# Kernel tuning notes

Hardware: AMD Instinct MI355X
Metric: run time of the kernel (lower is better)

Reference implementation:

```python
import jax, jax.numpy as jnp
import numpy as np

BATCH, C, BOX = 8, 1, 160
N, L = 20, 20


def setup_inputs() -> dict:
    key = jax.random.key(0)
    k1, k2, k3 = jax.random.split(key, 3)
    x = jax.random.normal(k1, (BATCH, C, BOX, BOX), dtype=jnp.float32)
    basis = jax.random.normal(k2, (N, L, 2, BOX, BOX), dtype=jnp.float32)
    angles = jax.random.uniform(k3, (BATCH,), dtype=jnp.float32) * (2.0 * np.pi)
    return {"x": x, "basis": basis, "angles": angles}


def reference(x, basis, angles):
    # euclid2basis: linear basis projection (GEMM in disguise)
    # coeffs: [b, c, N, L, 2]
    coeffs = jnp.einsum('bcij,nlrij->bcnlr', x, basis)

    # rotate: complex rotation of angular modes, angle scaled by harmonic index l
    l_mult = jnp.arange(L, dtype=x.dtype)                  # [L]
    ang = angles[:, None, None, None] * l_mult             # [b, 1, 1, L]
    ca, sa = jnp.cos(ang), jnp.sin(ang)
    a = coeffs[..., 0] * ca + coeffs[..., 1] * sa
    b = coeffs[..., 1] * ca - coeffs[..., 0] * sa
    rot = jnp.stack([a, b], axis=-1)                       # [b, c, N, L, 2]

    # basis2euclid: reconstruction (transpose GEMM)
    out = jnp.einsum('bcnlr,nlrij->bcij', rot, basis)      # [b, c, H, W]
    return out
```

## Files before the change

kernel.cpp:

```cpp
#include <hip/hip_runtime.h>
#include <math.h>

#define BATCH   8
#define LDIM    20
#define PIX     25600
#define PIX4    6400
#define NLPAIRS 400
#define NLR     800

#define NLG     2
#define KSPLIT  5
#define SLICE   (PIX4 / KSPLIT)

#define RPIX    64
#define RKS     4
#define RKLEN   (NLR / RKS)

__global__ __launch_bounds__(256) void proj_kernel(
    const float* __restrict__ x,
    const float* __restrict__ basis,
    float* __restrict__ part)
{
    const int tid   = threadIdx.x;
    const int rbase = blockIdx.x * (NLG * 2);
    const int kbase = blockIdx.y * SLICE;

    const float4* __restrict__ r0 = (const float4*)(basis + (size_t)(rbase + 0) * PIX);
    const float4* __restrict__ r1 = (const float4*)(basis + (size_t)(rbase + 1) * PIX);
    const float4* __restrict__ r2 = (const float4*)(basis + (size_t)(rbase + 2) * PIX);
    const float4* __restrict__ r3 = (const float4*)(basis + (size_t)(rbase + 3) * PIX);
    const float4* __restrict__ x4 = (const float4*)x;

    float acc[4][BATCH];
    #pragma unroll
    for (int r = 0; r < 4; ++r)
        #pragma unroll
        for (int b = 0; b < BATCH; ++b) acc[r][b] = 0.0f;

    #pragma unroll
    for (int it = 0; it < SLICE / 256; ++it) {
        const int i = kbase + it * 256 + tid;
        float4 b0 = r0[i];
        float4 b1 = r1[i];
        float4 b2 = r2[i];
        float4 b3 = r3[i];
        #pragma unroll
        for (int b = 0; b < BATCH; ++b) {
            float4 xv = x4[(size_t)b * PIX4 + i];
            acc[0][b] = fmaf(b0.x, xv.x, acc[0][b]);
            acc[0][b] = fmaf(b0.y, xv.y, acc[0][b]);
            acc[0][b] = fmaf(b0.z, xv.z, acc[0][b]);
            acc[0][b] = fmaf(b0.w, xv.w, acc[0][b]);
            acc[1][b] = fmaf(b1.x, xv.x, acc[1][b]);
            acc[1][b] = fmaf(b1.y, xv.y, acc[1][b]);
            acc[1][b] = fmaf(b1.z, xv.z, acc[1][b]);
            acc[1][b] = fmaf(b1.w, xv.w, acc[1][b]);
            acc[2][b] = fmaf(b2.x, xv.x, acc[2][b]);
            acc[2][b] = fmaf(b2.y, xv.y, acc[2][b]);
            acc[2][b] = fmaf(b2.z, xv.z, acc[2][b]);
            acc[2][b] = fmaf(b2.w, xv.w, acc[2][b]);
            acc[3][b] = fmaf(b3.x, xv.x, acc[3][b]);
            acc[3][b] = fmaf(b3.y, xv.y, acc[3][b]);
            acc[3][b] = fmaf(b3.z, xv.z, acc[3][b]);
            acc[3][b] = fmaf(b3.w, xv.w, acc[3][b]);
        }
    }

    #pragma unroll
    for (int r = 0; r < 4; ++r)
        #pragma unroll
        for (int b = 0; b < BATCH; ++b)
            #pragma unroll
            for (int off = 32; off > 0; off >>= 1)
                acc[r][b] += __shfl_down(acc[r][b], off);

    __shared__ float red[4][32];
    const int wave = tid >> 6;
    const int lane = tid & 63;
    if (lane == 0) {
        #pragma unroll
        for (int r = 0; r < 4; ++r)
            #pragma unroll
            for (int b = 0; b < BATCH; ++b)
                red[wave][r * BATCH + b] = acc[r][b];
    }
    __syncthreads();

    if (tid < 32) {
        const int r = tid >> 3;
        const int b = tid & 7;
        float v = red[0][tid] + red[1][tid] + red[2][tid] + red[3][tid];
        part[((size_t)blockIdx.y * NLR + rbase + r) * BATCH + b] = v;
    }
}

__global__ __launch_bounds__(256) void recon_kernel(
    const float* __restrict__ basis,
    const float* __restrict__ part,
    const float* __restrict__ angles,
    float* __restrict__ out)
{
    __shared__ float rl[NLR * BATCH];
    __shared__ float red[RKS - 1][RPIX][BATCH];
    __shared__ float cst[LDIM * BATCH], snt[LDIM * BATCH];

    const int tid = threadIdx.x;

    if (tid < LDIM * BATCH) {
        const int l = tid >> 3;
        const int b = tid & 7;
        __sincosf(angles[b] * (float)l, &snt[tid], &cst[tid]);
    }
    __syncthreads();

    for (int idx = tid; idx < NLR * BATCH; idx += 256) {
        const int nlr = idx >> 3;
        const int b   = idx & 7;
        float self = 0.0f, other = 0.0f;
        #pragma unroll
        for (int s = 0; s < KSPLIT; ++s) {
            self  += part[((size_t)s * NLR + nlr) * BATCH + b];
            other += part[((size_t)s * NLR + (nlr ^ 1)) * BATCH + b];
        }
        const int l  = (nlr >> 1) % LDIM;
        const float ca = cst[l * BATCH + b];
        const float sa = snt[l * BATCH + b];
        rl[idx] = (nlr & 1) == 0 ? fmaf(self, ca, other * sa)
                                 : fmaf(self, ca, -other * sa);
    }
    __syncthreads();

    const int lane = tid & 63;
    const int ks   = tid >> 6;
    const int pix  = blockIdx.x * RPIX + lane;

    float acc[BATCH];
    #pragma unroll
    for (int b = 0; b < BATCH; ++b) acc[b] = 0.0f;

    const float* __restrict__ bp = basis + (size_t)(ks * RKLEN) * PIX + pix;
    const float* __restrict__ rp = &rl[(ks * RKLEN) * BATCH];

    #pragma unroll 10
    for (int k = 0; k < RKLEN; ++k) {
        float bv = bp[(size_t)k * PIX];
        float4 v0 = *(const float4*)&rp[k * BATCH];
        float4 v1 = *(const float4*)&rp[k * BATCH + 4];
        acc[0] = fmaf(bv, v0.x, acc[0]);
        acc[1] = fmaf(bv, v0.y, acc[1]);
        acc[2] = fmaf(bv, v0.z, acc[2]);
        acc[3] = fmaf(bv, v0.w, acc[3]);
        acc[4] = fmaf(bv, v1.x, acc[4]);
        acc[5] = fmaf(bv, v1.y, acc[5]);
        acc[6] = fmaf(bv, v1.z, acc[6]);
        acc[7] = fmaf(bv, v1.w, acc[7]);
    }

    if (ks > 0) {
        #pragma unroll
        for (int b = 0; b < BATCH; ++b)
            red[ks - 1][lane][b] = acc[b];
    }
    __syncthreads();

    if (ks == 0) {
        #pragma unroll
        for (int w = 0; w < RKS - 1; ++w)
            #pragma unroll
            for (int b = 0; b < BATCH; ++b)
                acc[b] += red[w][lane][b];
        #pragma unroll
        for (int b = 0; b < BATCH; ++b)
            out[(size_t)b * PIX + pix] = acc[b];
    }
}

extern "C" void kernel_launch(void* const* d_in, const int* in_sizes, int n_in,
                              void* d_out, int out_size, void* d_ws, size_t ws_size,
                              hipStream_t stream) {
    (void)in_sizes; (void)n_in; (void)ws_size; (void)out_size;

    const float* x      = (const float*)d_in[0];
    const float* basis  = (const float*)d_in[1];
    const float* angles = (const float*)d_in[2];
    float* out  = (float*)d_out;
    float* part = (float*)d_ws;

    proj_kernel<<<dim3(NLPAIRS / NLG, KSPLIT), dim3(256), 0, stream>>>(x, basis, part);
    recon_kernel<<<dim3(PIX / RPIX), dim3(256), 0, stream>>>(basis, part, angles, out);
}
```

Baseline: 42.12 us.

## Split rotation into its own kernel and widen recon K-split to 8 waves

Moves the partial-sum reduction and the sincos rotation out of the reconstruction kernel into a small separate kernel, so each of the 400 recon blocks no longer redoes that work; recon blocks now just copy the rotated coefficients into shared memory. The recon kernel doubles to 512 threads with an 8-way K split for more memory-level parallelism, and the shared reduction buffer is transposed to avoid bank conflicts. In exchange it adds an extra kernel launch and a global round-trip for the rotated coefficients.

```diff
diff --git a/kernel.cpp b/kernel.cpp
--- a/kernel.cpp
+++ b/kernel.cpp
@@ -13,7 +13,7 @@
 #define SLICE   (PIX4 / KSPLIT)
 
 #define RPIX    64
-#define RKS     4
+#define RKS     8
 #define RKLEN   (NLR / RKS)
 
 __global__ __launch_bounds__(256) void proj_kernel(
@@ -94,40 +94,40 @@
     }
 }
 
-__global__ __launch_bounds__(256) void recon_kernel(
-    const float* __restrict__ basis,
+__global__ __launch_bounds__(256) void rotate_kernel(
     const float* __restrict__ part,
     const float* __restrict__ angles,
+    float* __restrict__ rot)
+{
+    const int idx = blockIdx.x * 256 + threadIdx.x;
+    const int nlr = idx >> 3;
+    const int b   = idx & 7;
+
+    float self = 0.0f, other = 0.0f;
+    #pragma unroll
+    for (int s = 0; s < KSPLIT; ++s) {
+        self  += part[((size_t)s * NLR + nlr) * BATCH + b];
+        other += part[((size_t)s * NLR + (nlr ^ 1)) * BATCH + b];
+    }
+    const int l = (nlr >> 1) % LDIM;
+    float ca, sa;
+    __sincosf(angles[b] * (float)l, &sa, &ca);
+    rot[idx] = (nlr & 1) == 0 ? fmaf(self, ca, other * sa)
+                              : fmaf(self, ca, -other * sa);
+}
+
+__global__ __launch_bounds__(512) void recon_kernel(
+    const float* __restrict__ basis,
+    const float* __restrict__ rot,
     float* __restrict__ out)
 {
     __shared__ float rl[NLR * BATCH];
-    __shared__ float red[RKS - 1][RPIX][BATCH];
-    __shared__ float cst[LDIM * BATCH], snt[LDIM * BATCH];
+    __shared__ float red[RKS - 1][BATCH][RPIX];
 
     const int tid = threadIdx.x;
 
-    if (tid < LDIM * BATCH) {
-        const int l = tid >> 3;
-        const int b = tid & 7;
-        __sincosf(angles[b] * (float)l, &snt[tid], &cst[tid]);
-    }
-    __syncthreads();
-
-    for (int idx = tid; idx < NLR * BATCH; idx += 256) {
-        const int nlr = idx >> 3;
-        const int b   = idx & 7;
-        float self = 0.0f, other = 0.0f;
-        #pragma unroll
-        for (int s = 0; s < KSPLIT; ++s) {
-            self  += part[((size_t)s * NLR + nlr) * BATCH + b];
-            other += part[((size_t)s * NLR + (nlr ^ 1)) * BATCH + b];
-        }
-        const int l  = (nlr >> 1) % LDIM;
-        const float ca = cst[l * BATCH + b];
-        const float sa = snt[l * BATCH + b];
-        rl[idx] = (nlr & 1) == 0 ? fmaf(self, ca, other * sa)
-                                 : fmaf(self, ca, -other * sa);
-    }
+    for (int idx = tid; idx < NLR * BATCH; idx += 512)
+        rl[idx] = rot[idx];
     __syncthreads();
 
     const int lane = tid & 63;
@@ -159,7 +159,7 @@
     if (ks > 0) {
         #pragma unroll
         for (int b = 0; b < BATCH; ++b)
-            red[ks - 1][lane][b] = acc[b];
+            red[ks - 1][b][lane] = acc[b];
     }
     __syncthreads();
 
@@ -168,7 +168,7 @@
         for (int w = 0; w < RKS - 1; ++w)
             #pragma unroll
             for (int b = 0; b < BATCH; ++b)
-                acc[b] += red[w][lane][b];
+                acc[b] += red[w][b][lane];
         #pragma unroll
         for (int b = 0; b < BATCH; ++b)
             out[(size_t)b * PIX + pix] = acc[b];
@@ -185,7 +185,9 @@
     const float* angles = (const float*)d_in[2];
     float* out  = (float*)d_out;
     float* part = (float*)d_ws;
+    float* rot  = part + (size_t)KSPLIT * NLR * BATCH;
 
     proj_kernel<<<dim3(NLPAIRS / NLG, KSPLIT), dim3(256), 0, stream>>>(x, basis, part);
-    recon_kernel<<<dim3(PIX / RPIX), dim3(256), 0, stream>>>(basis, part, angles, out);
+    rotate_kernel<<<dim3(NLR * BATCH / 256), dim3(256), 0, stream>>>(part, angles, rot);
+    recon_kernel<<<dim3(PIX / RPIX), dim3(512), 0, stream>>>(basis, rot, out);
 }
```

New measurement: 41.76 us. Within noise of the previous version (-0.9%).
